# Kernel tuning notes

Measured on AMD Instinct MI355X. Metric: run time of the kernel, lower is better.

Reference implementation:

```python
import jax, jax.numpy as jnp
import numpy as np

B = 4096          # batch_size * world_size
D = 256           # embedding dim
TEMP = 0.5        # temperature
EPS = 1e-8        # torch CosineSimilarity eps


def setup_inputs() -> dict:
    key = jax.random.key(0)
    k1, k2 = jax.random.split(key)
    z_i = jax.random.normal(k1, (B, D), dtype=jnp.float32)
    z_j = jax.random.normal(k2, (B, D), dtype=jnp.float32)
    return {"z_i": z_i, "z_j": z_j}


def reference(z_i, z_j):
    N = 2 * B
    z = jnp.concatenate([z_i, z_j], axis=0)                      # [N, D]
    # Cosine similarity: normalize rows (clamped norm like torch eps), then matmul.
    norms = jnp.maximum(jnp.linalg.norm(z, axis=1, keepdims=True), EPS)
    zn = z / norms
    sim = jnp.matmul(zn, zn.T) / TEMP                            # [N, N]
    # Positive pairs: offsets +B and -B from the diagonal.
    pos = jnp.concatenate([jnp.diagonal(sim, B), jnp.diagonal(sim, -B)])  # [N]
    # Cross-entropy with label 0 over [pos, negatives]:
    # logsumexp over {pos} U {negatives} == logsumexp over row excluding the diagonal
    # (the (i, i±B) entries removed by the mask are exactly re-added as the positive).
    neg_inf = jnp.array(-jnp.inf, dtype=sim.dtype)
    sim_nodiag = jnp.where(jnp.eye(N, dtype=bool), neg_inf, sim)
    lse = jax.nn.logsumexp(sim_nodiag, axis=1)                   # [N]
    loss = jnp.sum(lse - pos) / N                                # reduction='sum' then /N
    return loss
```

## Files before the change

kernel.cpp:

```cpp
#include <hip/hip_runtime.h>

#define NROWS 8192
#define DIM   256
#define BHALF 4096
#define NCHUNK 8
#define SCALE 1.69864358f
#define LN2F  0.69314718f

typedef unsigned char u8;
typedef __attribute__((ext_vector_type(4))) float f32x4;
typedef __attribute__((ext_vector_type(4))) int   i32x4;
typedef __attribute__((ext_vector_type(8))) int   i32x8;

__device__ inline void gload_lds16(const void* g, void* l) {
  __builtin_amdgcn_global_load_lds(
      (const __attribute__((address_space(1))) void*)g,
      (__attribute__((address_space(3))) void*)l, 16, 0, 0);
}

__global__ __launch_bounds__(256) void nrm_kernel(const float* __restrict__ zi,
                                                  const float* __restrict__ zj,
                                                  u8* __restrict__ zn8,
                                                  float* __restrict__ out) {
  if (blockIdx.x == 0 && threadIdx.x == 0) out[0] = 0.f;
  const int w = threadIdx.x >> 6, l = threadIdx.x & 63;
  const int row = blockIdx.x * 4 + w;
  const float* src = (row < BHALF) ? zi + (size_t)row * DIM
                                   : zj + (size_t)(row - BHALF) * DIM;
  float4 v = *(const float4*)(src + l * 4);
  float ss = v.x * v.x + v.y * v.y + v.z * v.z + v.w * v.w;
#pragma unroll
  for (int m = 1; m < 64; m <<= 1) ss += __shfl_xor(ss, m);
  float inv = SCALE / fmaxf(sqrtf(ss), 1e-8f);
  int p = __builtin_amdgcn_cvt_pk_fp8_f32(v.x * inv, v.y * inv, 0, false);
  p = __builtin_amdgcn_cvt_pk_fp8_f32(v.z * inv, v.w * inv, p, true);
  *(int*)(zn8 + (size_t)row * DIM + (size_t)l * 4) = p;
}

__global__ __launch_bounds__(256, 2) void sim_kernel(const u8* __restrict__ zn8,
                                                     float* __restrict__ partials,
                                                     float* __restrict__ pos) {
  __shared__ __align__(16) u8 Bsm[2][128 * DIM];
  __shared__ float plane[2][128];

  const int t = threadIdx.x;
  const int w = t >> 6, l = t & 63;
  const int wa = w >> 1, wb = w & 1;
  const int rl = l & 15, kg = l >> 4;

  const int rp = (int)blockIdx.x >> 3;
  const int ch = (int)blockIdx.x & 7;
  const int colbase = ch * 1024;

  auto STAGE = [&](int base_row, u8* dst) {
#pragma unroll
    for (int i = 0; i < 8; ++i) {
      int c = i * 256 + t;
      int r = c >> 4, cd = c & 15;
      int cs = (cd & 8) | ((cd ^ r) & 7);
      gload_lds16(zn8 + (size_t)(base_row + r) * DIM + (size_t)cs * 16,
                  dst + (size_t)((i * 256 + w * 64) * 16));
    }
  };
  auto RD2 = [&](const u8* buf, int row, i32x8* dst) {
    const int salt = row & 7;
    const u8* base = buf + row * DIM;
#pragma unroll
    for (int k = 0; k < 2; ++k) {
      i32x4 lo = *(const i32x4*)(base + ((k * 8 + ((kg * 2) ^ salt)) << 4));
      i32x4 hi = *(const i32x4*)(base + ((k * 8 + ((kg * 2 + 1) ^ salt)) << 4));
      dst[k] = __builtin_shufflevector(lo, hi, 0, 1, 2, 3, 4, 5, 6, 7);
    }
  };

  STAGE(rp * 128, &Bsm[0][0]);
  STAGE(colbase, &Bsm[1][0]);
  asm volatile("s_waitcnt vmcnt(8)" ::: "memory");
  __builtin_amdgcn_sched_barrier(0);
  __builtin_amdgcn_s_barrier();
  __builtin_amdgcn_sched_barrier(0);

  i32x8 pb[4][2];
#pragma unroll
  for (int pj = 0; pj < 4; ++pj)
    RD2(&Bsm[0][0], wb * 64 + pj * 16 + rl, pb[pj]);
  asm volatile("s_waitcnt lgkmcnt(0)" ::: "memory");
  __builtin_amdgcn_sched_barrier(0);

  const int dtile = ((rp >> 3) == ch) ? (rp & 7) : -1;
  const int pg = (rp < 32) ? (rp + 32) : (rp - 32);
  const int ptile = ((pg >> 3) == ch) ? (pg & 7) : -1;

  float rsum[4] = {0.f, 0.f, 0.f, 0.f};
  float pv[4]   = {0.f, 0.f, 0.f, 0.f};
  const bool dlane = (wa == wb) && (kg == (rl >> 2));

#pragma unroll 2
  for (int ti = 0; ti < 8; ++ti) {
    asm volatile("s_waitcnt vmcnt(0)" ::: "memory");
    __builtin_amdgcn_sched_barrier(0);
    __builtin_amdgcn_s_barrier();
    __builtin_amdgcn_sched_barrier(0);

    const u8* Bb = &Bsm[(ti + 1) & 1][0];
    if (ti < 7) STAGE(colbase + (ti + 1) * 128, &Bsm[ti & 1][0]);

    const bool tdiag = (ti == dtile), tpos = (ti == ptile);

    i32x8 af[2][2];
    RD2(Bb, wa * 64 + rl, af[0]);
#pragma unroll
    for (int ci = 0; ci < 4; ++ci) {
      if (ci < 3) RD2(Bb, wa * 64 + (ci + 1) * 16 + rl, af[(ci + 1) & 1]);
      if (ci < 3) asm volatile("s_waitcnt lgkmcnt(4)" ::: "memory");
      else        asm volatile("s_waitcnt lgkmcnt(0)" ::: "memory");
      __builtin_amdgcn_sched_barrier(0);

      f32x4 acc[4];
#pragma unroll
      for (int pj = 0; pj < 4; ++pj) acc[pj] = (f32x4){0.f, 0.f, 0.f, 0.f};
      __builtin_amdgcn_s_setprio(1);
#pragma unroll
      for (int k = 0; k < 2; ++k)
#pragma unroll
        for (int pj = 0; pj < 4; ++pj)
          acc[pj] = __builtin_amdgcn_mfma_scale_f32_16x16x128_f8f6f4(
              af[ci & 1][k], pb[pj][k], acc[pj],
              0, 0,
              0, 0x7f7f7f7f,
              0, 0x7f7f7f7f);
      __builtin_amdgcn_s_setprio(0);

#pragma unroll
      for (int pj = 0; pj < 4; ++pj)
#pragma unroll
        for (int jj = 0; jj < 4; ++jj)
          rsum[pj] += __builtin_amdgcn_exp2f(acc[pj][jj]);
      if (tdiag && dlane)
        rsum[ci] -= __builtin_amdgcn_exp2f(acc[ci][rl & 3]);
      if (tpos && dlane) pv[ci] = acc[ci][rl & 3];
    }
  }

#pragma unroll
  for (int pj = 0; pj < 4; ++pj) {
    rsum[pj] += __shfl_xor(rsum[pj], 16);
    rsum[pj] += __shfl_xor(rsum[pj], 32);
  }
  if (kg == 0) {
#pragma unroll
    for (int pj = 0; pj < 4; ++pj)
      plane[wa][wb * 64 + pj * 16 + rl] = rsum[pj];
  }
  __syncthreads();
  if (t < 128)
    partials[(size_t)ch * NROWS + rp * 128 + t] = plane[0][t] + plane[1][t];
  if (ptile >= 0 && dlane) {
#pragma unroll
    for (int ci = 0; ci < 4; ++ci)
      pos[rp * 128 + wb * 64 + ci * 16 + rl] = pv[ci] * LN2F;
  }
}

__global__ __launch_bounds__(256) void fin_kernel(const float* __restrict__ partials,
                                                  const float* __restrict__ pos,
                                                  float* __restrict__ out) {
  const int r = blockIdx.x * 256 + threadIdx.x;
  float s = 0.f;
#pragma unroll
  for (int ch = 0; ch < NCHUNK; ++ch) s += partials[(size_t)ch * NROWS + r];
  float v = logf(s) - pos[r];
#pragma unroll
  for (int m = 1; m < 64; m <<= 1) v += __shfl_xor(v, m);
  __shared__ float wsum[4];
  const int w = threadIdx.x >> 6, l = threadIdx.x & 63;
  if (l == 0) wsum[w] = v;
  __syncthreads();
  if (threadIdx.x == 0)
    atomicAdd(out, (wsum[0] + wsum[1] + wsum[2] + wsum[3]) * (1.f / NROWS));
}

extern "C" void kernel_launch(void* const* d_in, const int* in_sizes, int n_in,
                              void* d_out, int out_size, void* d_ws, size_t ws_size,
                              hipStream_t stream) {
  const float* zi = (const float*)d_in[0];
  const float* zj = (const float*)d_in[1];

  u8*    zn8      = (u8*)d_ws;
  float* partials = (float*)((char*)d_ws + (size_t)NROWS * DIM);
  float* pos      = (float*)((char*)partials + (size_t)NCHUNK * NROWS * 4);
  float* out      = (float*)d_out;

  nrm_kernel<<<NROWS / 4, 256, 0, stream>>>(zi, zj, zn8, out);
  sim_kernel<<<64 * NCHUNK, 256, 0, stream>>>(zn8, partials, pos);
  fin_kernel<<<NROWS / 256, 256, 0, stream>>>(partials, pos, out);
}
```

Baseline: 32.27 us.

## Split sim kernel into 16 column chunks with 64-row tiles for higher occupancy

```diff
diff --git a/kernel.cpp b/kernel.cpp
--- a/kernel.cpp
+++ b/kernel.cpp
@@ -3,7 +3,7 @@
 #define NROWS 8192
 #define DIM   256
 #define BHALF 4096
-#define NCHUNK 8
+#define NCHUNK 16
 #define SCALE 1.69864358f
 #define LN2F  0.69314718f
 
@@ -37,10 +37,10 @@
   *(int*)(zn8 + (size_t)row * DIM + (size_t)l * 4) = p;
 }
 
-__global__ __launch_bounds__(256, 2) void sim_kernel(const u8* __restrict__ zn8,
+__global__ __launch_bounds__(256, 4) void sim_kernel(const u8* __restrict__ zn8,
                                                      float* __restrict__ partials,
                                                      float* __restrict__ pos) {
-  __shared__ __align__(16) u8 Bsm[2][128 * DIM];
+  __shared__ __align__(16) u8 Bsm[2][64 * DIM];
   __shared__ float plane[2][128];
 
   const int t = threadIdx.x;
@@ -48,11 +48,11 @@
   const int wa = w >> 1, wb = w & 1;
   const int rl = l & 15, kg = l >> 4;
 
-  const int rp = (int)blockIdx.x >> 3;
-  const int ch = (int)blockIdx.x & 7;
-  const int colbase = ch * 1024;
-
-  auto STAGE = [&](int base_row, u8* dst) {
+  const int rp = (int)blockIdx.x >> 4;
+  const int ch = (int)blockIdx.x & 15;
+  const int colbase = ch * 512;
+
+  auto STAGE_P = [&](int base_row, u8* dst) {
 #pragma unroll
     for (int i = 0; i < 8; ++i) {
       int c = i * 256 + t;
@@ -62,6 +62,16 @@
                   dst + (size_t)((i * 256 + w * 64) * 16));
     }
   };
+  auto STAGE_T = [&](int base_row, u8* dst) {
+#pragma unroll
+    for (int i = 0; i < 4; ++i) {
+      int c = i * 256 + t;
+      int r = c >> 4, cd = c & 15;
+      int cs = (cd & 8) | ((cd ^ r) & 7);
+      gload_lds16(zn8 + (size_t)(base_row + r) * DIM + (size_t)cs * 16,
+                  dst + (size_t)((i * 256 + w * 64) * 16));
+    }
+  };
   auto RD2 = [&](const u8* buf, int row, i32x8* dst) {
     const int salt = row & 7;
     const u8* base = buf + row * DIM;
@@ -73,9 +83,8 @@
     }
   };
 
-  STAGE(rp * 128, &Bsm[0][0]);
-  STAGE(colbase, &Bsm[1][0]);
-  asm volatile("s_waitcnt vmcnt(8)" ::: "memory");
+  STAGE_P(rp * 128, &Bsm[0][0]);
+  asm volatile("s_waitcnt vmcnt(0)" ::: "memory");
   __builtin_amdgcn_sched_barrier(0);
   __builtin_amdgcn_s_barrier();
   __builtin_amdgcn_sched_barrier(0);
@@ -86,14 +95,18 @@
     RD2(&Bsm[0][0], wb * 64 + pj * 16 + rl, pb[pj]);
   asm volatile("s_waitcnt lgkmcnt(0)" ::: "memory");
   __builtin_amdgcn_sched_barrier(0);
-
-  const int dtile = ((rp >> 3) == ch) ? (rp & 7) : -1;
-  const int pg = (rp < 32) ? (rp + 32) : (rp - 32);
-  const int ptile = ((pg >> 3) == ch) ? (pg & 7) : -1;
+  __builtin_amdgcn_s_barrier();
+  __builtin_amdgcn_sched_barrier(0);
+  STAGE_T(colbase, &Bsm[1][0]);
+
+  const int dg  = rp * 2 + wb;
+  const int ptg = dg + ((rp < 32) ? 64 : -64);
+  const int dt = ((dg >> 3) == ch)  ? (dg & 7)  : -1;
+  const int pt = ((ptg >> 3) == ch) ? (ptg & 7) : -1;
+  const bool dlane = (kg == (rl >> 2));
 
   float rsum[4] = {0.f, 0.f, 0.f, 0.f};
-  float pv[4]   = {0.f, 0.f, 0.f, 0.f};
-  const bool dlane = (wa == wb) && (kg == (rl >> 2));
+  float pv[2]   = {0.f, 0.f};
 
 #pragma unroll 2
   for (int ti = 0; ti < 8; ++ti) {
@@ -103,17 +116,15 @@
     __builtin_amdgcn_sched_barrier(0);
 
     const u8* Bb = &Bsm[(ti + 1) & 1][0];
-    if (ti < 7) STAGE(colbase + (ti + 1) * 128, &Bsm[ti & 1][0]);
-
-    const bool tdiag = (ti == dtile), tpos = (ti == ptile);
-
-    i32x8 af[2][2];
-    RD2(Bb, wa * 64 + rl, af[0]);
-#pragma unroll
-    for (int ci = 0; ci < 4; ++ci) {
-      if (ci < 3) RD2(Bb, wa * 64 + (ci + 1) * 16 + rl, af[(ci + 1) & 1]);
-      if (ci < 3) asm volatile("s_waitcnt lgkmcnt(4)" ::: "memory");
-      else        asm volatile("s_waitcnt lgkmcnt(0)" ::: "memory");
+    if (ti < 7) STAGE_T(colbase + (ti + 1) * 64, &Bsm[ti & 1][0]);
+
+    const bool tdiag = (ti == dt), tpos = (ti == pt);
+
+#pragma unroll
+    for (int ci = 0; ci < 2; ++ci) {
+      i32x8 af[2];
+      RD2(Bb, wa * 32 + ci * 16 + rl, af);
+      asm volatile("s_waitcnt lgkmcnt(0)" ::: "memory");
       __builtin_amdgcn_sched_barrier(0);
 
       f32x4 acc[4];
@@ -125,7 +136,7 @@
 #pragma unroll
         for (int pj = 0; pj < 4; ++pj)
           acc[pj] = __builtin_amdgcn_mfma_scale_f32_16x16x128_f8f6f4(
-              af[ci & 1][k], pb[pj][k], acc[pj],
+              af[k], pb[pj][k], acc[pj],
               0, 0,
               0, 0x7f7f7f7f,
               0, 0x7f7f7f7f);
@@ -136,9 +147,10 @@
 #pragma unroll
         for (int jj = 0; jj < 4; ++jj)
           rsum[pj] += __builtin_amdgcn_exp2f(acc[pj][jj]);
+      const int pjs = wa * 2 + ci;
       if (tdiag && dlane)
-        rsum[ci] -= __builtin_amdgcn_exp2f(acc[ci][rl & 3]);
-      if (tpos && dlane) pv[ci] = acc[ci][rl & 3];
+        rsum[pjs] -= __builtin_amdgcn_exp2f(acc[pjs][rl & 3]);
+      if (tpos && dlane) pv[ci] = acc[pjs][rl & 3];
     }
   }
 
@@ -155,10 +167,10 @@
   __syncthreads();
   if (t < 128)
     partials[(size_t)ch * NROWS + rp * 128 + t] = plane[0][t] + plane[1][t];
-  if (ptile >= 0 && dlane) {
-#pragma unroll
-    for (int ci = 0; ci < 4; ++ci)
-      pos[rp * 128 + wb * 64 + ci * 16 + rl] = pv[ci] * LN2F;
+  if (pt >= 0 && dlane) {
+#pragma unroll
+    for (int ci = 0; ci < 2; ++ci)
+      pos[rp * 128 + wb * 64 + (wa * 2 + ci) * 16 + rl] = pv[ci] * LN2F;
   }
 }
 
```

After: 38.21 us. +18.4%, slower.

## Switch similarity tiles to 32x32x64 FP8 MFMA with per-wave 32-column strips

Applied to the files above, without the earlier changes.

```diff
diff --git a/kernel.cpp b/kernel.cpp
--- a/kernel.cpp
+++ b/kernel.cpp
@@ -8,7 +8,7 @@
 #define LN2F  0.69314718f
 
 typedef unsigned char u8;
-typedef __attribute__((ext_vector_type(4))) float f32x4;
+typedef __attribute__((ext_vector_type(16))) float f32x16;
 typedef __attribute__((ext_vector_type(4))) int   i32x4;
 typedef __attribute__((ext_vector_type(8))) int   i32x8;
 
@@ -41,12 +41,11 @@
                                                      float* __restrict__ partials,
                                                      float* __restrict__ pos) {
   __shared__ __align__(16) u8 Bsm[2][128 * DIM];
-  __shared__ float plane[2][128];
+  __shared__ float plane[4][128];
 
   const int t = threadIdx.x;
   const int w = t >> 6, l = t & 63;
-  const int wa = w >> 1, wb = w & 1;
-  const int rl = l & 15, kg = l >> 4;
+  const int n31 = l & 31, kh = l >> 5;
 
   const int rp = (int)blockIdx.x >> 3;
   const int ch = (int)blockIdx.x & 7;
@@ -62,15 +61,13 @@
                   dst + (size_t)((i * 256 + w * 64) * 16));
     }
   };
-  auto RD2 = [&](const u8* buf, int row, i32x8* dst) {
+  auto RD32 = [&](const u8* buf, int row, int kk) -> i32x8 {
     const int salt = row & 7;
     const u8* base = buf + row * DIM;
-#pragma unroll
-    for (int k = 0; k < 2; ++k) {
-      i32x4 lo = *(const i32x4*)(base + ((k * 8 + ((kg * 2) ^ salt)) << 4));
-      i32x4 hi = *(const i32x4*)(base + ((k * 8 + ((kg * 2 + 1) ^ salt)) << 4));
-      dst[k] = __builtin_shufflevector(lo, hi, 0, 1, 2, 3, 4, 5, 6, 7);
-    }
+    const int c0 = kk * 4 + kh * 2;
+    i32x4 lo = *(const i32x4*)(base + (((c0 & 8) | ((c0 ^ salt) & 7)) << 4));
+    i32x4 hi = *(const i32x4*)(base + ((((c0 + 1) & 8) | (((c0 + 1) ^ salt) & 7)) << 4));
+    return __builtin_shufflevector(lo, hi, 0, 1, 2, 3, 4, 5, 6, 7);
   };
 
   STAGE(rp * 128, &Bsm[0][0]);
@@ -80,22 +77,24 @@
   __builtin_amdgcn_s_barrier();
   __builtin_amdgcn_sched_barrier(0);
 
-  i32x8 pb[4][2];
+  i32x8 pb[4][4];
 #pragma unroll
   for (int pj = 0; pj < 4; ++pj)
-    RD2(&Bsm[0][0], wb * 64 + pj * 16 + rl, pb[pj]);
+#pragma unroll
+    for (int kk = 0; kk < 4; ++kk)
+      pb[pj][kk] = RD32(&Bsm[0][0], pj * 32 + n31, kk);
   asm volatile("s_waitcnt lgkmcnt(0)" ::: "memory");
   __builtin_amdgcn_sched_barrier(0);
 
-  const int dtile = ((rp >> 3) == ch) ? (rp & 7) : -1;
+  const int dt = ((rp >> 3) == ch) ? (rp & 7) : -1;
   const int pg = (rp < 32) ? (rp + 32) : (rp - 32);
-  const int ptile = ((pg >> 3) == ch) ? (pg & 7) : -1;
+  const int pt = ((pg >> 3) == ch) ? (pg & 7) : -1;
+  const bool dsel = (((l >> 2) & 1) == kh);
+  const int regsel = (l & 3) | (((l >> 3) & 3) << 2);
 
   float rsum[4] = {0.f, 0.f, 0.f, 0.f};
-  float pv[4]   = {0.f, 0.f, 0.f, 0.f};
-  const bool dlane = (wa == wb) && (kg == (rl >> 2));
-
-#pragma unroll 2
+  float pv = 0.f;
+
   for (int ti = 0; ti < 8; ++ti) {
     asm volatile("s_waitcnt vmcnt(0)" ::: "memory");
     __builtin_amdgcn_sched_barrier(0);
@@ -105,61 +104,81 @@
     const u8* Bb = &Bsm[(ti + 1) & 1][0];
     if (ti < 7) STAGE(colbase + (ti + 1) * 128, &Bsm[ti & 1][0]);
 
-    const bool tdiag = (ti == dtile), tpos = (ti == ptile);
-
-    i32x8 af[2][2];
-    RD2(Bb, wa * 64 + rl, af[0]);
-#pragma unroll
-    for (int ci = 0; ci < 4; ++ci) {
-      if (ci < 3) RD2(Bb, wa * 64 + (ci + 1) * 16 + rl, af[(ci + 1) & 1]);
-      if (ci < 3) asm volatile("s_waitcnt lgkmcnt(4)" ::: "memory");
-      else        asm volatile("s_waitcnt lgkmcnt(0)" ::: "memory");
+    f32x16 acc[4];
+#pragma unroll
+    for (int pj = 0; pj < 4; ++pj) acc[pj] = (f32x16)(0.f);
+
+    i32x8 af0 = RD32(Bb, w * 32 + n31, 0);
+    i32x8 af1;
+#pragma unroll
+    for (int kk = 0; kk < 4; ++kk) {
+      if (kk < 3) {
+        i32x8 nxt = RD32(Bb, w * 32 + n31, kk + 1);
+        if (kk & 1) af0 = nxt; else af1 = nxt;
+        asm volatile("s_waitcnt lgkmcnt(2)" ::: "memory");
+      } else {
+        asm volatile("s_waitcnt lgkmcnt(0)" ::: "memory");
+      }
       __builtin_amdgcn_sched_barrier(0);
-
-      f32x4 acc[4];
-#pragma unroll
-      for (int pj = 0; pj < 4; ++pj) acc[pj] = (f32x4){0.f, 0.f, 0.f, 0.f};
+      const i32x8 a = (kk & 1) ? af1 : af0;
       __builtin_amdgcn_s_setprio(1);
 #pragma unroll
-      for (int k = 0; k < 2; ++k)
-#pragma unroll
-        for (int pj = 0; pj < 4; ++pj)
-          acc[pj] = __builtin_amdgcn_mfma_scale_f32_16x16x128_f8f6f4(
-              af[ci & 1][k], pb[pj][k], acc[pj],
-              0, 0,
-              0, 0x7f7f7f7f,
-              0, 0x7f7f7f7f);
+      for (int pj = 0; pj < 4; ++pj)
+        acc[pj] = __builtin_amdgcn_mfma_scale_f32_32x32x64_f8f6f4(
+            a, pb[pj][kk], acc[pj],
+            0, 0,
+            0, 0x7f7f7f7f,
+            0, 0x7f7f7f7f);
       __builtin_amdgcn_s_setprio(0);
-
+    }
+
+#pragma unroll
+    for (int pj = 0; pj < 4; ++pj) {
+      float e0 = 0.f, e1 = 0.f, e2 = 0.f, e3 = 0.f;
+#pragma unroll
+      for (int r16 = 0; r16 < 16; r16 += 4) {
+        e0 += __builtin_amdgcn_exp2f(acc[pj][r16]);
+        e1 += __builtin_amdgcn_exp2f(acc[pj][r16 + 1]);
+        e2 += __builtin_amdgcn_exp2f(acc[pj][r16 + 2]);
+        e3 += __builtin_amdgcn_exp2f(acc[pj][r16 + 3]);
+      }
+      rsum[pj] += (e0 + e1) + (e2 + e3);
+    }
+    if (ti == dt && dsel) {
 #pragma unroll
       for (int pj = 0; pj < 4; ++pj)
-#pragma unroll
-        for (int jj = 0; jj < 4; ++jj)
-          rsum[pj] += __builtin_amdgcn_exp2f(acc[pj][jj]);
-      if (tdiag && dlane)
-        rsum[ci] -= __builtin_amdgcn_exp2f(acc[ci][rl & 3]);
-      if (tpos && dlane) pv[ci] = acc[ci][rl & 3];
+        if (pj == w) {
+          float sv = acc[pj][0];
+#pragma unroll
+          for (int r16 = 1; r16 < 16; ++r16)
+            sv = (regsel == r16) ? acc[pj][r16] : sv;
+          rsum[pj] -= __builtin_amdgcn_exp2f(sv);
+        }
+    }
+    if (ti == pt && dsel) {
+#pragma unroll
+      for (int pj = 0; pj < 4; ++pj)
+        if (pj == w) {
+          float sv = acc[pj][0];
+#pragma unroll
+          for (int r16 = 1; r16 < 16; ++r16)
+            sv = (regsel == r16) ? acc[pj][r16] : sv;
+          pv = sv;
+        }
     }
   }
 
 #pragma unroll
   for (int pj = 0; pj < 4; ++pj) {
-    rsum[pj] += __shfl_xor(rsum[pj], 16);
     rsum[pj] += __shfl_xor(rsum[pj], 32);
-  }
-  if (kg == 0) {
-#pragma unroll
-    for (int pj = 0; pj < 4; ++pj)
-      plane[wa][wb * 64 + pj * 16 + rl] = rsum[pj];
+    if (l < 32) plane[w][pj * 32 + l] = rsum[pj];
   }
   __syncthreads();
   if (t < 128)
-    partials[(size_t)ch * NROWS + rp * 128 + t] = plane[0][t] + plane[1][t];
-  if (ptile >= 0 && dlane) {
-#pragma unroll
-    for (int ci = 0; ci < 4; ++ci)
-      pos[rp * 128 + wb * 64 + ci * 16 + rl] = pv[ci] * LN2F;
-  }
+    partials[(size_t)ch * NROWS + rp * 128 + t] =
+        (plane[0][t] + plane[1][t]) + (plane[2][t] + plane[3][t]);
+  if (pt >= 0 && dsel)
+    pos[rp * 128 + w * 32 + n31] = pv * LN2F;
 }
 
 __global__ __launch_bounds__(256) void fin_kernel(const float* __restrict__ partials,
```

Result: slower. 34.41 us (+6.6%).

## Software-pipeline exp epilogue behind next MFMA batch and precompute stage offsets

Applied to the files above, without the earlier changes.

```diff
diff --git a/kernel.cpp b/kernel.cpp
--- a/kernel.cpp
+++ b/kernel.cpp
@@ -52,15 +52,19 @@
   const int ch = (int)blockIdx.x & 7;
   const int colbase = ch * 1024;
 
+  int soff[8], doff[8];
+#pragma unroll
+  for (int i = 0; i < 8; ++i) {
+    int c = i * 256 + t;
+    int r = c >> 4, cd = c & 15;
+    int cs = (cd & 8) | ((cd ^ r) & 7);
+    soff[i] = r * DIM + cs * 16;
+    doff[i] = (i * 256 + w * 64) * 16;
+  }
   auto STAGE = [&](int base_row, u8* dst) {
 #pragma unroll
-    for (int i = 0; i < 8; ++i) {
-      int c = i * 256 + t;
-      int r = c >> 4, cd = c & 15;
-      int cs = (cd & 8) | ((cd ^ r) & 7);
-      gload_lds16(zn8 + (size_t)(base_row + r) * DIM + (size_t)cs * 16,
-                  dst + (size_t)((i * 256 + w * 64) * 16));
-    }
+    for (int i = 0; i < 8; ++i)
+      gload_lds16(zn8 + (size_t)base_row * DIM + soff[i], dst + doff[i]);
   };
   auto RD2 = [&](const u8* buf, int row, i32x8* dst) {
     const int salt = row & 7;
@@ -94,6 +98,7 @@
   float rsum[4] = {0.f, 0.f, 0.f, 0.f};
   float pv[4]   = {0.f, 0.f, 0.f, 0.f};
   const bool dlane = (wa == wb) && (kg == (rl >> 2));
+  const f32x4 z4 = {0.f, 0.f, 0.f, 0.f};
 
 #pragma unroll 2
   for (int ti = 0; ti < 8; ++ti) {
@@ -107,6 +112,18 @@
 
     const bool tdiag = (ti == dtile), tpos = (ti == ptile);
 
+    auto EPI = [&](int cip, const f32x4* a) {
+#pragma unroll
+      for (int pj = 0; pj < 4; ++pj)
+#pragma unroll
+        for (int jj = 0; jj < 4; ++jj)
+          rsum[pj] += __builtin_amdgcn_exp2f(a[pj][jj]);
+      if (tdiag && dlane)
+        rsum[cip] -= __builtin_amdgcn_exp2f(a[cip][rl & 3]);
+      if (tpos && dlane) pv[cip] = a[cip][rl & 3];
+    };
+
+    f32x4 acc[2][4];
     i32x8 af[2][2];
     RD2(Bb, wa * 64 + rl, af[0]);
 #pragma unroll
@@ -116,30 +133,23 @@
       else        asm volatile("s_waitcnt lgkmcnt(0)" ::: "memory");
       __builtin_amdgcn_sched_barrier(0);
 
-      f32x4 acc[4];
-#pragma unroll
-      for (int pj = 0; pj < 4; ++pj) acc[pj] = (f32x4){0.f, 0.f, 0.f, 0.f};
       __builtin_amdgcn_s_setprio(1);
 #pragma unroll
-      for (int k = 0; k < 2; ++k)
-#pragma unroll
-        for (int pj = 0; pj < 4; ++pj)
-          acc[pj] = __builtin_amdgcn_mfma_scale_f32_16x16x128_f8f6f4(
-              af[ci & 1][k], pb[pj][k], acc[pj],
-              0, 0,
-              0, 0x7f7f7f7f,
-              0, 0x7f7f7f7f);
+      for (int pj = 0; pj < 4; ++pj)
+        acc[ci & 1][pj] = __builtin_amdgcn_mfma_scale_f32_16x16x128_f8f6f4(
+            af[ci & 1][0], pb[pj][0], z4,
+            0, 0, 0, 0x7f7f7f7f, 0, 0x7f7f7f7f);
+#pragma unroll
+      for (int pj = 0; pj < 4; ++pj)
+        acc[ci & 1][pj] = __builtin_amdgcn_mfma_scale_f32_16x16x128_f8f6f4(
+            af[ci & 1][1], pb[pj][1], acc[ci & 1][pj],
+            0, 0, 0, 0x7f7f7f7f, 0, 0x7f7f7f7f);
       __builtin_amdgcn_s_setprio(0);
-
-#pragma unroll
-      for (int pj = 0; pj < 4; ++pj)
-#pragma unroll
-        for (int jj = 0; jj < 4; ++jj)
-          rsum[pj] += __builtin_amdgcn_exp2f(acc[pj][jj]);
-      if (tdiag && dlane)
-        rsum[ci] -= __builtin_amdgcn_exp2f(acc[ci][rl & 3]);
-      if (tpos && dlane) pv[ci] = acc[ci][rl & 3];
+      __builtin_amdgcn_sched_barrier(0);
+
+      if (ci > 0) EPI(ci - 1, acc[(ci - 1) & 1]);
     }
+    EPI(3, acc[1]);
   }
 
 #pragma unroll
```

Result: no change. 32.07 us (-0.6%).
